# Optimization experiments

Measured on AMD Instinct MI355X. Metric: run time of the kernel, lower is better.

The kernel has to match this reference:

```python
import jax, jax.numpy as jnp
import numpy as np

N = 117000   # vocab / number of WordNet synsets (square adjacency)
E = 500000   # number of COO edges
B, T = 4, 64 # batch, seq len


def setup_inputs() -> dict:
    key = jax.random.key(0)
    k1, k2, k3, k4 = jax.random.split(key, 4)
    logits = jax.random.normal(k1, (B, T, N), dtype=jnp.float32)
    # ensure every row index appears at least once so row-normalization never divides by zero
    row = jnp.concatenate([jnp.arange(N, dtype=jnp.int32),
                           jax.random.randint(k2, (E - N,), 0, N, dtype=jnp.int32)])
    col = jax.random.randint(k3, (E,), 0, N, dtype=jnp.int32)
    edge_index = jnp.stack([row, col], axis=0)  # [2, E]
    vv = jax.random.uniform(k4, (E,), dtype=jnp.float32, minval=0.1, maxval=1.0)
    return {"logits": logits, "vv": vv, "edge_index": edge_index}


def reference(logits, vv, edge_index):
    # StructuredLogits.forward with DEHARDCODE_ALPHA=1.0, renormalize=True:
    #   neighbors = spmm(A, logits_flat^T)^T ; neighbors /= row_sum ; out = neighbors + logits
    row, col = edge_index[0], edge_index[1]
    n = logits.shape[-1]
    x = logits.reshape(-1, n).T                              # [N, BT]
    contrib = vv[:, None] * x[col]                           # [E, BT] gather + scale
    neigh_T = jax.ops.segment_sum(contrib, row, num_segments=n)   # [N, BT] scatter-add (SpMM)
    row_sum = jax.ops.segment_sum(vv, row, num_segments=n)        # [N] row-normalizer
    neighbors = (neigh_T / row_sum[:, None]).T.reshape(logits.shape)
    return neighbors + logits
```

## Files before the change

### kernel.cpp

```cpp
#include <hip/hip_runtime.h>
#include <hip/hip_fp16.h>

#define NN 117000
#define BT 256

#define SCAN_CHUNK 1024
#define SCAN_NB ((NN + SCAN_CHUNK - 1) / SCAN_CHUNK)
#define SCAN_P2_T 128

union U8 { uint2 u; __half2 h[2]; };


__global__ void hist_kernel(const int* __restrict__ row, int* __restrict__ count, int E) {
    int e = blockIdx.x * blockDim.x + threadIdx.x;
    if (e < E) atomicAdd(&count[row[e]], 1);
}

__global__ void scan_phase1(const int* __restrict__ count, int* __restrict__ block_sums) {
    __shared__ int s[256];
    int base = blockIdx.x * SCAN_CHUNK + threadIdx.x * 4;
    int sum = 0;
#pragma unroll
    for (int j = 0; j < 4; ++j) {
        int idx = base + j;
        if (idx < NN) sum += count[idx];
    }
    s[threadIdx.x] = sum;
    __syncthreads();
    for (int off = 128; off > 0; off >>= 1) {
        if (threadIdx.x < off) s[threadIdx.x] += s[threadIdx.x + off];
        __syncthreads();
    }
    if (threadIdx.x == 0) block_sums[blockIdx.x] = s[0];
}

__global__ void scan_phase2(int* __restrict__ block_sums, int* __restrict__ row_ptr) {
    __shared__ int s[SCAN_P2_T];
    int t = threadIdx.x;
    int v = (t < SCAN_NB) ? block_sums[t] : 0;
    s[t] = v;
    __syncthreads();
    for (int off = 1; off < SCAN_P2_T; off <<= 1) {
        int u = (t >= off) ? s[t - off] : 0;
        __syncthreads();
        s[t] += u;
        __syncthreads();
    }
    if (t < SCAN_NB) block_sums[t] = (t == 0) ? 0 : s[t - 1];
    if (t == SCAN_P2_T - 1) row_ptr[NN] = s[SCAN_NB - 1];
}

__global__ void scan_phase3(int* __restrict__ row_ptr, const int* __restrict__ block_offs,
                            int* __restrict__ cursor) {
    __shared__ int s[256];
    int base = blockIdx.x * SCAN_CHUNK + threadIdx.x * 4;
    int v[4];
    int sum = 0;
#pragma unroll
    for (int j = 0; j < 4; ++j) {
        int idx = base + j;
        v[j] = (idx < NN) ? row_ptr[idx] : 0;
        sum += v[j];
    }
    s[threadIdx.x] = sum;
    __syncthreads();
    for (int off = 1; off < 256; off <<= 1) {
        int u = (threadIdx.x >= off) ? s[threadIdx.x - off] : 0;
        __syncthreads();
        s[threadIdx.x] += u;
        __syncthreads();
    }
    int prefix = block_offs[blockIdx.x] + ((threadIdx.x == 0) ? 0 : s[threadIdx.x - 1]);
#pragma unroll
    for (int j = 0; j < 4; ++j) {
        int idx = base + j;
        if (idx < NN) {
            row_ptr[idx] = prefix;
            cursor[idx]  = prefix;
            prefix += v[j];
        }
    }
}

__global__ void scatter_kernel(const int* __restrict__ row, const int* __restrict__ col,
                               const float* __restrict__ vv, int* __restrict__ cursor,
                               int2* __restrict__ edge_s, int E) {
    int e = blockIdx.x * blockDim.x + threadIdx.x;
    if (e >= E) return;
    int p = atomicAdd(&cursor[row[e]], 1);
    edge_s[p] = make_int2(col[e], __float_as_int(vv[e]));
}


__global__ void transpose_h_kernel(const float* __restrict__ logits, __half* __restrict__ xT) {
    __shared__ float s[64][33];
    int tx = threadIdx.x & 31;
    int ty = threadIdx.x >> 5;
    int i0  = blockIdx.x * 32;
    int bt0 = blockIdx.y * 64;
    int i = i0 + tx;
    if (i < NN) {
#pragma unroll
        for (int r = 0; r < 8; ++r) {
            int bt = bt0 + ty + r * 8;
            s[ty + r * 8][tx] = logits[(size_t)bt * NN + i];
        }
    }
    __syncthreads();
#pragma unroll
    for (int r = 0; r < 4; ++r) {
        int il = ty + r * 8;
        int i2 = i0 + il;
        if (i2 < NN) {
            __half2 h = __floats2half2_rn(s[2 * tx][il], s[2 * tx + 1][il]);
            ((__half2*)(xT + (size_t)i2 * BT + bt0))[tx] = h;
        }
    }
}

__global__ void row_gather_kernel(const int* __restrict__ row_ptr,
                                  const int2* __restrict__ edge_s,
                                  const __half* __restrict__ xT,
                                  __half* __restrict__ accT) {
    int i = blockIdx.x * 4 + (threadIdx.x >> 6);
    if (i >= NN) return;
    int lane = threadIdx.x & 63;
    int k0 = row_ptr[i], k1 = row_ptr[i + 1];
    const uint2* xT2 = (const uint2*)xT;
    float4 acc = make_float4(0.f, 0.f, 0.f, 0.f);
    float rs = 0.f;
    for (int kb = k0; kb < k1; kb += 64) {
        int nk = min(64, k1 - kb);
        int2 ed = make_int2(0, 0);
        if (lane < nk) ed = edge_s[kb + lane];
        int   ccol = ed.x;
        float cval = __int_as_float(ed.y);
        int c0 = __shfl(ccol, 0);
        uint2 cur = xT2[(size_t)c0 * (BT / 4) + lane];
        for (int j = 0; j < nk; ++j) {
            uint2 nxt = make_uint2(0u, 0u);
            if (j + 1 < nk) {
                int cn = __shfl(ccol, j + 1);
                nxt = xT2[(size_t)cn * (BT / 4) + lane];
            }
            float v = __shfl(cval, j);
            rs += v;
            U8 t; t.u = cur;
            float2 fa = __half22float2(t.h[0]);
            float2 fb = __half22float2(t.h[1]);
            acc.x += v * fa.x; acc.y += v * fa.y;
            acc.z += v * fb.x; acc.w += v * fb.y;
            cur = nxt;
        }
    }
    float inv = (rs > 0.f) ? (1.0f / rs) : 0.f;
    U8 o;
    o.h[0] = __floats2half2_rn(acc.x * inv, acc.y * inv);
    o.h[1] = __floats2half2_rn(acc.z * inv, acc.w * inv);
    ((uint2*)accT)[(size_t)i * (BT / 4) + lane] = o.u;
}

__global__ void finalize_kernel(const float* __restrict__ logits, const __half* __restrict__ accT,
                                float* __restrict__ out) {
    __shared__ float s[32][65];
    int tx = threadIdx.x & 31;
    int ty = threadIdx.x >> 5;
    int i0  = blockIdx.x * 32;
    int bt0 = blockIdx.y * 64;
#pragma unroll
    for (int r = 0; r < 4; ++r) {
        int il = ty + r * 8;
        int i = i0 + il;
        if (i < NN) {
            __half2 h = ((const __half2*)(accT + (size_t)i * BT + bt0))[tx];
            float2 f = __half22float2(h);
            s[il][2 * tx]     = f.x;
            s[il][2 * tx + 1] = f.y;
        }
    }
    __syncthreads();
#pragma unroll
    for (int r = 0; r < 8; ++r) {
        int bt = bt0 + ty + r * 8;
        int i = i0 + tx;
        if (i < NN) {
            size_t idx = (size_t)bt * NN + i;
            out[idx] = logits[idx] + s[tx][bt - bt0];
        }
    }
}


__global__ void transpose_kernel(const float* __restrict__ logits, float* __restrict__ xT) {
    __shared__ float s[32][33];
    int tx = threadIdx.x & 31;
    int ty = threadIdx.x >> 5;
    int i0  = blockIdx.x * 32;
    int bt0 = blockIdx.y * 32;
    int i = i0 + tx;
#pragma unroll
    for (int r = 0; r < 4; ++r) {
        int bt = bt0 + ty + r * 8;
        if (i < NN) s[ty + r * 8][tx] = logits[(size_t)bt * NN + i];
    }
    __syncthreads();
#pragma unroll
    for (int r = 0; r < 4; ++r) {
        int i2 = i0 + ty + r * 8;
        if (i2 < NN) xT[(size_t)i2 * BT + bt0 + tx] = s[tx][ty + r * 8];
    }
}

__global__ void rowsum_kernel(const int* __restrict__ row, const float* __restrict__ vv,
                              float* __restrict__ row_sum, int E) {
    int e = blockIdx.x * blockDim.x + threadIdx.x;
    if (e < E) atomicAdd(&row_sum[row[e]], vv[e]);
}

__global__ void edge_kernel(const int* __restrict__ row, const int* __restrict__ col,
                            const float* __restrict__ vv, const float* __restrict__ xT,
                            float* __restrict__ acc, int E) {
    int e = blockIdx.x * 4 + (threadIdx.x >> 6);
    if (e >= E) return;
    int lane = threadIdx.x & 63;
    int r = row[e];
    int c = col[e];
    float v = vv[e];
    float4 x4 = ((const float4*)(xT + (size_t)c * BT))[lane];
    float* dst = acc + (size_t)r * BT + lane * 4;
    atomicAdd(dst + 0, v * x4.x);
    atomicAdd(dst + 1, v * x4.y);
    atomicAdd(dst + 2, v * x4.z);
    atomicAdd(dst + 3, v * x4.w);
}

__global__ void finalize_div_kernel(const float* __restrict__ logits, const float* __restrict__ acc,
                                    const float* __restrict__ row_sum, float* __restrict__ out) {
    __shared__ float s[32][33];
    __shared__ float rs[32];
    int tx = threadIdx.x & 31;
    int ty = threadIdx.x >> 5;
    int i0  = blockIdx.x * 32;
    int bt0 = blockIdx.y * 32;
#pragma unroll
    for (int r = 0; r < 4; ++r) {
        int il = ty + r * 8;
        int i = i0 + il;
        if (i < NN) s[il][tx] = acc[(size_t)i * BT + bt0 + tx];
    }
    if (threadIdx.x < 32) {
        int i = i0 + (int)threadIdx.x;
        rs[threadIdx.x] = (i < NN) ? row_sum[i] : 1.0f;
    }
    __syncthreads();
#pragma unroll
    for (int r = 0; r < 4; ++r) {
        int bt = bt0 + ty + r * 8;
        int i = i0 + tx;
        if (i < NN) {
            size_t idx = (size_t)bt * NN + i;
            out[idx] = logits[idx] + s[tx][ty + r * 8] / rs[tx];
        }
    }
}

extern "C" void kernel_launch(void* const* d_in, const int* in_sizes, int n_in,
                              void* d_out, int out_size, void* d_ws, size_t ws_size,
                              hipStream_t stream) {
    const float* logits = (const float*)d_in[0];
    const float* vv     = (const float*)d_in[1];
    const int*   ei     = (const int*)d_in[2];
    const int E = in_sizes[1];
    const int* row = ei;
    const int* col = ei + E;
    float* out = (float*)d_out;

    const size_t accN = (size_t)NN * BT;

    const int e_blocks   = (E + 255) / 256;
    const int row_blocks = (NN + 3) / 4;

    const size_t need_csr = (size_t)E * sizeof(int2)
                          + 2 * accN * sizeof(__half)
                          + (size_t)(NN + 1 + NN + SCAN_NB) * sizeof(int);

    if (ws_size >= need_csr) {
        int2*   edge_s     = (int2*)d_ws;
        __half* xT         = (__half*)(edge_s + E);
        __half* accT       = xT + accN;
        int*    row_ptr    = (int*)(accT + accN);
        int*    cursor     = row_ptr + (NN + 1);
        int*    block_sums = cursor + NN;

        dim3 tgrid((NN + 31) / 32, BT / 64);

        hipMemsetAsync(row_ptr, 0, (NN + 1) * sizeof(int), stream);
        hist_kernel<<<e_blocks, 256, 0, stream>>>(row, row_ptr, E);
        scan_phase1<<<SCAN_NB, 256, 0, stream>>>(row_ptr, block_sums);
        scan_phase2<<<1, SCAN_P2_T, 0, stream>>>(block_sums, row_ptr);
        scan_phase3<<<SCAN_NB, 256, 0, stream>>>(row_ptr, block_sums, cursor);
        scatter_kernel<<<e_blocks, 256, 0, stream>>>(row, col, vv, cursor, edge_s, E);
        transpose_h_kernel<<<tgrid, 256, 0, stream>>>(logits, xT);
        row_gather_kernel<<<row_blocks, 256, 0, stream>>>(row_ptr, edge_s, xT, accT);
        finalize_kernel<<<tgrid, 256, 0, stream>>>(logits, accT, out);
    } else {
        float* acc     = (float*)d_ws;
        float* xT      = acc + accN;
        float* row_sum = xT + accN;
        dim3 tgrid32((NN + 31) / 32, BT / 32);
        hipMemsetAsync(acc, 0, accN * sizeof(float), stream);
        hipMemsetAsync(row_sum, 0, NN * sizeof(float), stream);
        rowsum_kernel<<<e_blocks, 256, 0, stream>>>(row, vv, row_sum, E);
        transpose_kernel<<<tgrid32, 256, 0, stream>>>(logits, xT);
        edge_kernel<<<(E + 3) / 4, 256, 0, stream>>>(row, col, vv, xT, acc, E);
        finalize_div_kernel<<<tgrid32, 256, 0, stream>>>(logits, acc, row_sum, out);
    }
}
```

Before: 400.5 us.

## Fuse row gather with finalize via LDS transpose, dropping fp16 accT buffer

Merges the CSR row-gather SpMM and the finalize/transpose kernel into one kernel. Each 512-thread block computes 32 rows into LDS in fp32, then transposes and adds logits when writing out. This removes the fp16 intermediate write and reread and one kernel launch, and also avoids fp16 rounding of the result. The cost is that each wave now handles 4 rows serially, with a larger LDS footprint that may lower occupancy and latency hiding for the gather.

```diff
diff --git a/kernel.cpp b/kernel.cpp
--- a/kernel.cpp
+++ b/kernel.cpp
@@ -7,6 +7,9 @@
 #define SCAN_CHUNK 1024
 #define SCAN_NB ((NN + SCAN_CHUNK - 1) / SCAN_CHUNK)
 #define SCAN_P2_T 128
+
+#define ROWS_PB 32
+#define LDS_STRIDE (BT + 2)
 
 union U8 { uint2 u; __half2 h[2]; };
 
@@ -118,74 +121,66 @@
     }
 }
 
-__global__ void row_gather_kernel(const int* __restrict__ row_ptr,
-                                  const int2* __restrict__ edge_s,
-                                  const __half* __restrict__ xT,
-                                  __half* __restrict__ accT) {
-    int i = blockIdx.x * 4 + (threadIdx.x >> 6);
-    if (i >= NN) return;
+__global__ void row_gather_fused_kernel(const int* __restrict__ row_ptr,
+                                        const int2* __restrict__ edge_s,
+                                        const __half* __restrict__ xT,
+                                        const float* __restrict__ logits,
+                                        float* __restrict__ out) {
+    __shared__ float s[ROWS_PB][LDS_STRIDE];
+    int wave = threadIdx.x >> 6;
     int lane = threadIdx.x & 63;
-    int k0 = row_ptr[i], k1 = row_ptr[i + 1];
+    int i0 = blockIdx.x * ROWS_PB;
     const uint2* xT2 = (const uint2*)xT;
-    float4 acc = make_float4(0.f, 0.f, 0.f, 0.f);
-    float rs = 0.f;
-    for (int kb = k0; kb < k1; kb += 64) {
-        int nk = min(64, k1 - kb);
-        int2 ed = make_int2(0, 0);
-        if (lane < nk) ed = edge_s[kb + lane];
-        int   ccol = ed.x;
-        float cval = __int_as_float(ed.y);
-        int c0 = __shfl(ccol, 0);
-        uint2 cur = xT2[(size_t)c0 * (BT / 4) + lane];
-        for (int j = 0; j < nk; ++j) {
-            uint2 nxt = make_uint2(0u, 0u);
-            if (j + 1 < nk) {
-                int cn = __shfl(ccol, j + 1);
-                nxt = xT2[(size_t)cn * (BT / 4) + lane];
+
+#pragma unroll
+    for (int rr = 0; rr < 4; ++rr) {
+        int r_local = wave * 4 + rr;
+        int i = i0 + r_local;
+        if (i < NN) {
+            int k0 = row_ptr[i], k1 = row_ptr[i + 1];
+            float4 acc = make_float4(0.f, 0.f, 0.f, 0.f);
+            float rs = 0.f;
+            for (int kb = k0; kb < k1; kb += 64) {
+                int nk = min(64, k1 - kb);
+                int2 ed = make_int2(0, 0);
+                if (lane < nk) ed = edge_s[kb + lane];
+                int   ccol = ed.x;
+                float cval = __int_as_float(ed.y);
+                int c0 = __shfl(ccol, 0);
+                uint2 cur = xT2[(size_t)c0 * (BT / 4) + lane];
+                for (int j = 0; j < nk; ++j) {
+                    uint2 nxt = make_uint2(0u, 0u);
+                    if (j + 1 < nk) {
+                        int cn = __shfl(ccol, j + 1);
+                        nxt = xT2[(size_t)cn * (BT / 4) + lane];
+                    }
+                    float v = __shfl(cval, j);
+                    rs += v;
+                    U8 t; t.u = cur;
+                    float2 fa = __half22float2(t.h[0]);
+                    float2 fb = __half22float2(t.h[1]);
+                    acc.x += v * fa.x; acc.y += v * fa.y;
+                    acc.z += v * fb.x; acc.w += v * fb.y;
+                    cur = nxt;
+                }
             }
-            float v = __shfl(cval, j);
-            rs += v;
-            U8 t; t.u = cur;
-            float2 fa = __half22float2(t.h[0]);
-            float2 fb = __half22float2(t.h[1]);
-            acc.x += v * fa.x; acc.y += v * fa.y;
-            acc.z += v * fb.x; acc.w += v * fb.y;
-            cur = nxt;
-        }
-    }
-    float inv = (rs > 0.f) ? (1.0f / rs) : 0.f;
-    U8 o;
-    o.h[0] = __floats2half2_rn(acc.x * inv, acc.y * inv);
-    o.h[1] = __floats2half2_rn(acc.z * inv, acc.w * inv);
-    ((uint2*)accT)[(size_t)i * (BT / 4) + lane] = o.u;
-}
-
-__global__ void finalize_kernel(const float* __restrict__ logits, const __half* __restrict__ accT,
-                                float* __restrict__ out) {
-    __shared__ float s[32][65];
+            float inv = (rs > 0.f) ? (1.0f / rs) : 0.f;
+            float2* sp = (float2*)&s[r_local][lane * 4];
+            sp[0] = make_float2(acc.x * inv, acc.y * inv);
+            sp[1] = make_float2(acc.z * inv, acc.w * inv);
+        }
+    }
+    __syncthreads();
+
     int tx = threadIdx.x & 31;
     int ty = threadIdx.x >> 5;
-    int i0  = blockIdx.x * 32;
-    int bt0 = blockIdx.y * 64;
-#pragma unroll
-    for (int r = 0; r < 4; ++r) {
-        int il = ty + r * 8;
-        int i = i0 + il;
-        if (i < NN) {
-            __half2 h = ((const __half2*)(accT + (size_t)i * BT + bt0))[tx];
-            float2 f = __half22float2(h);
-            s[il][2 * tx]     = f.x;
-            s[il][2 * tx + 1] = f.y;
-        }
-    }
-    __syncthreads();
-#pragma unroll
-    for (int r = 0; r < 8; ++r) {
-        int bt = bt0 + ty + r * 8;
-        int i = i0 + tx;
-        if (i < NN) {
+    int i = i0 + tx;
+    if (i < NN) {
+#pragma unroll
+        for (int r = 0; r < 16; ++r) {
+            int bt = r * 16 + ty;
             size_t idx = (size_t)bt * NN + i;
-            out[idx] = logits[idx] + s[tx][bt - bt0];
+            out[idx] = logits[idx] + s[tx][bt];
         }
     }
 }
@@ -277,22 +272,21 @@
 
     const size_t accN = (size_t)NN * BT;
 
-    const int e_blocks   = (E + 255) / 256;
-    const int row_blocks = (NN + 3) / 4;
+    const int e_blocks = (E + 255) / 256;
 
     const size_t need_csr = (size_t)E * sizeof(int2)
-                          + 2 * accN * sizeof(__half)
+                          + accN * sizeof(__half)
                           + (size_t)(NN + 1 + NN + SCAN_NB) * sizeof(int);
 
     if (ws_size >= need_csr) {
         int2*   edge_s     = (int2*)d_ws;
         __half* xT         = (__half*)(edge_s + E);
-        __half* accT       = xT + accN;
-        int*    row_ptr    = (int*)(accT + accN);
+        int*    row_ptr    = (int*)(xT + accN);
         int*    cursor     = row_ptr + (NN + 1);
         int*    block_sums = cursor + NN;
 
         dim3 tgrid((NN + 31) / 32, BT / 64);
+        const int fuse_blocks = (NN + ROWS_PB - 1) / ROWS_PB;
 
         hipMemsetAsync(row_ptr, 0, (NN + 1) * sizeof(int), stream);
         hist_kernel<<<e_blocks, 256, 0, stream>>>(row, row_ptr, E);
@@ -301,8 +295,8 @@
         scan_phase3<<<SCAN_NB, 256, 0, stream>>>(row_ptr, block_sums, cursor);
         scatter_kernel<<<e_blocks, 256, 0, stream>>>(row, col, vv, cursor, edge_s, E);
         transpose_h_kernel<<<tgrid, 256, 0, stream>>>(logits, xT);
-        row_gather_kernel<<<row_blocks, 256, 0, stream>>>(row_ptr, edge_s, xT, accT);
-        finalize_kernel<<<tgrid, 256, 0, stream>>>(logits, accT, out);
+        row_gather_fused_kernel<<<fuse_blocks, 512, 0, stream>>>(row_ptr, edge_s, xT,
+                                                                 logits, out);
     } else {
         float* acc     = (float*)d_ws;
         float* xT      = acc + accN;
```

Result: faster. 377.8 us (-5.7%).
